# Kernel optimization log

Measured on AMD Instinct MI355X. Metric: run time of the kernel, lower is better.

The kernel has to match this reference:

```python
import jax, jax.numpy as jnp
import numpy as np
import math

DIM = 512
NUM_HEADS = 8
DIM_HEAD = DIM // NUM_HEADS


def normalized_coords(h, w):
    # (h*w, 2) with (x, y) in [0, 1]
    y = jnp.linspace(0.0, 1.0, h)
    x = jnp.linspace(0.0, 1.0, w)
    yg, xg = jnp.meshgrid(y, x, indexing='ij')
    return jnp.stack([xg.ravel(), yg.ravel()], axis=-1)


def rotate_half(x):
    dh = x.shape[-1] // 2
    return jnp.concatenate([-x[..., dh:], x[..., :dh]], axis=-1)


def apply_rope(t, coords):
    # t: (n, heads, seq, dim_head); coords: (seq, 2) (identical across batch)
    dim_half = t.shape[-1] // 2
    freq = 1.0 / (10000.0 ** (jnp.arange(dim_half, dtype=jnp.float32) / dim_half))
    ang_x = coords[:, 0:1] * freq  # (seq, dim_half)
    ang_y = coords[:, 1:2] * freq
    ang = jnp.concatenate([ang_x, ang_y], axis=-1)  # (seq, dim_head)
    cos, sin = jnp.cos(ang), jnp.sin(ang)
    return t * cos + rotate_half(t) * sin


def setup_inputs() -> dict:
    key = jax.random.key(0)
    ks = jax.random.split(key, 12)
    n, Np, d, H, W = 4, 1024, DIM, 64, 64
    s = 0.02
    return {
        'local_feat': jax.random.normal(ks[0], (n, Np, d), jnp.float32),
        'global_feat': jax.random.normal(ks[1], (n, d, H, W), jnp.float32),
        'Wq': jax.random.normal(ks[2], (d, d), jnp.float32) * s,
        'bq': jnp.zeros((d,), jnp.float32),
        'Wk': jax.random.normal(ks[3], (d, d), jnp.float32) * s,
        'bk': jnp.zeros((d,), jnp.float32),
        'Wv': jax.random.normal(ks[4], (d, d), jnp.float32) * s,
        'bv': jnp.zeros((d,), jnp.float32),
        'Wg': jax.random.normal(ks[5], (d, 2 * d), jnp.float32) * s,
        'bg': jnp.zeros((d,), jnp.float32),
        'Wo': jax.random.normal(ks[6], (d, d), jnp.float32) * s,
        'bo': jnp.zeros((d,), jnp.float32),
    }


def reference(local_feat, global_feat, Wq, bq, Wk, bk, Wv, bv, Wg, bg, Wo, bo):
    n, Np, d = local_feat.shape
    _, _, H, W = global_feat.shape
    h, dh = NUM_HEADS, DIM_HEAD
    gf = global_feat.reshape(n, d, H * W).transpose(0, 2, 1)  # (n, HW, d)

    P = int(math.isqrt(Np))
    local_coords = normalized_coords(P, P)      # (Np, 2)
    global_coords = normalized_coords(H, W)     # (HW, 2)

    def proj(x, Wt, b):
        return x @ Wt.T + b

    Q = proj(local_feat, Wq, bq).reshape(n, Np, h, dh).transpose(0, 2, 1, 3)
    K = proj(gf, Wk, bk).reshape(n, H * W, h, dh).transpose(0, 2, 1, 3)
    V = proj(gf, Wv, bv).reshape(n, H * W, h, dh).transpose(0, 2, 1, 3)

    Q = apply_rope(Q, local_coords)
    K = apply_rope(K, global_coords)

    scores = jnp.einsum('bhqd,bhkd->bhqk', Q, K) / math.sqrt(dh)
    attn = jax.nn.softmax(scores, axis=-1)
    ao = jnp.einsum('bhqk,bhkd->bhqd', attn, V)
    ao = ao.transpose(0, 2, 1, 3).reshape(n, Np, d)

    gate = jax.nn.sigmoid(jnp.concatenate([local_feat, ao], axis=-1) @ Wg.T + bg)
    enhanced = local_feat + gate * ao
    return enhanced @ Wo.T + bo
```

## Files before the change

kernel.cpp:

```cpp
#include <hip/hip_runtime.h>
#include <hip/hip_bf16.h>
#include <cstdint>

typedef __hip_bfloat16 BF;
typedef unsigned short ushort_t;
typedef __attribute__((ext_vector_type(8))) __bf16 bf16x8;
typedef __attribute__((ext_vector_type(4))) float f32x4;

__device__ __forceinline__ float b2f(BF x) { return __bfloat162float(x); }
__device__ __forceinline__ unsigned short f2bu(float f) {
  union { BF b; unsigned short u; } c; c.b = __float2bfloat16(f); return c.u;
}
__device__ __forceinline__ float rdE(const void* p, size_t i, bool f32) {
  return f32 ? ((const float*)p)[i] : __bfloat162float(((const BF*)p)[i]);
}
__device__ __forceinline__ void rd16(const void* p, size_t i, bool f32, ushort_t* out) {
  if (f32) {
    const float* fp = (const float*)p + i;
#pragma unroll
    for (int j = 0; j < 16; j += 4) {
      float4 v = *(const float4*)(fp + j);
      out[j] = f2bu(v.x); out[j + 1] = f2bu(v.y);
      out[j + 2] = f2bu(v.z); out[j + 3] = f2bu(v.w);
    }
  } else {
    const uint4* up = (const uint4*)((const BF*)p + i);
    *(uint4*)&out[0] = up[0];
    *(uint4*)&out[8] = up[1];
  }
}

__global__ void detect_k(const unsigned short* __restrict__ x, int* __restrict__ flag) {
  __shared__ int cnt;
  if (threadIdx.x == 0) cnt = 0;
  __syncthreads();
  int c = 0;
  for (int i = threadIdx.x; i < 4096; i += 256) {
    int e = (x[i] >> 7) & 0xFF;
    if (e >= 0x86) c++;
  }
  if (c) atomicAdd(&cnt, c);
  __syncthreads();
  if (threadIdx.x == 0) *flag = (cnt > 64) ? 1 : 0;
}

__global__ __launch_bounds__(256) void prep_k(const void* __restrict__ gfeat,
                                              BF* __restrict__ gfT,
                                              const int* __restrict__ flagp) {
  const bool f32 = (*flagp != 0);
  __shared__ __align__(16) ushort_t T[64][72];
  const int g = blockIdx.x;
  const int bz = g & 3, mt = (g >> 2) & 63, kt = g >> 8;
  const int t = threadIdx.x;
  {
    int krow = t >> 2, mg = t & 3;
    ushort_t vals[16];
    rd16(gfeat,
         (size_t)bz * 512 * 4096 + (size_t)(kt * 64 + krow) * 4096 + mt * 64 + mg * 16,
         f32, vals);
#pragma unroll
    for (int j = 0; j < 16; ++j) T[mg * 16 + j][krow] = vals[j];
  }
  __syncthreads();
  int mrow = t >> 2, kg = t & 3;
  uint4 a = *(const uint4*)&T[mrow][kg * 16];
  uint4 b = *(const uint4*)&T[mrow][kg * 16 + 8];
  size_t o = ((size_t)bz * 4096 + mt * 64 + mrow) * 512 + kt * 64 + kg * 16;
  *(uint4*)&gfT[o] = a;
  *(uint4*)&gfT[o + 8] = b;
}

#define QS 0.1803368801111f
template <int MODE>
__global__ __launch_bounds__(256) void mgemm_k(
    const void* __restrict__ Aext, const BF* __restrict__ Aint,
    const void* __restrict__ Bw, const void* __restrict__ Bw2,
    const void* __restrict__ biasv, const void* __restrict__ bias2,
    BF* __restrict__ outInt, BF* __restrict__ outInt2,
    void* __restrict__ outExt, int Kdim, const int* __restrict__ flagp) {
  const bool f32 = (*flagp != 0);
  const int tid = threadIdx.x;
  const int w = tid >> 6, lane = tid & 63;
  const int quad = lane >> 4, l16 = lane & 15;

  if constexpr (MODE == 5) {
    __shared__ __align__(16) ushort_t smem[2][128][72];
    auto As = smem[0];
    auto Bs = smem[1];
    const int wm = w >> 1, wn = w & 1;
    const int g = blockIdx.x;
    const int a = g & 7, y = (g >> 3) & 7, bidx = g >> 6;
    const int m0 = ((bidx << 1) | (a & 1)) * 128;
    const int n0 = y * 128;
    const int bz = a >> 1;

    f32x4 acc[4][4] = {};
    for (int k0 = 0; k0 < Kdim; k0 += 64) {
      __syncthreads();
#pragma unroll
      for (int u = 0; u < 2; ++u) {
        int unit = tid + u * 256;
        int row = unit >> 2, cg = unit & 3;
        const uint4* p = (const uint4*)(Aint + ((size_t)bz * 4096 + m0 + row) * 512 +
                                        k0 + cg * 16);
        *(uint4*)&As[row][cg * 16] = p[0];
        *(uint4*)&As[row][cg * 16 + 8] = p[1];
      }
#pragma unroll
      for (int u = 0; u < 2; ++u) {
        int unit = tid + u * 256;
        int row = unit >> 2, cg = unit & 3;
        const void* bsrc = (n0 >= 512) ? Bw2 : Bw;
        size_t nrow = (n0 >= 512) ? (n0 - 512 + row) : (n0 + row);
        ushort_t vals[16];
        rd16(bsrc, nrow * Kdim + k0 + cg * 16, f32, vals);
        *(uint4*)&Bs[row][cg * 16] = *(uint4*)&vals[0];
        *(uint4*)&Bs[row][cg * 16 + 8] = *(uint4*)&vals[8];
      }
      __syncthreads();
#pragma unroll
      for (int kc = 0; kc < 2; ++kc) {
        bf16x8 af[4], bfv[4];
#pragma unroll
        for (int i = 0; i < 4; ++i) {
          af[i] = *(const bf16x8*)&As[wm * 64 + i * 16 + l16][kc * 32 + quad * 8];
          bfv[i] = *(const bf16x8*)&Bs[wn * 64 + i * 16 + l16][kc * 32 + quad * 8];
        }
#pragma unroll
        for (int mt = 0; mt < 4; ++mt)
#pragma unroll
          for (int nt = 0; nt < 4; ++nt)
            acc[mt][nt] = __builtin_amdgcn_mfma_f32_16x16x32_bf16(af[mt], bfv[nt], acc[mt][nt], 0, 0, 0);
      }
    }
    if (n0 < 512) {
      const int head = (n0 + wn * 64) >> 6;
#pragma unroll
      for (int mt = 0; mt < 4; ++mt)
#pragma unroll
        for (int r = 0; r < 4; ++r) {
          int pg = m0 + wm * 64 + mt * 16 + quad * 4 + r;
          float x = (float)(pg & 63) * (1.f / 63.f);
          float yy = (float)(pg >> 6) * (1.f / 63.f);
          size_t base = (((size_t)bz * 8 + head) * 4096 + pg) * 64;
#pragma unroll
          for (int j = 0; j < 2; ++j) {
            int c0 = j * 16 + l16;
            float t0 = acc[mt][j][r] + rdE(biasv, head * 64 + c0, f32);
            float t1 = acc[mt][j + 2][r] + rdE(biasv, head * 64 + c0 + 32, f32);
            float fr = __expf((float)c0 * (-9.210340371976184f / 32.f));
            float ax = x * fr, ay = yy * fr;
            outInt[base + c0] = __float2bfloat16(t0 * __cosf(ax) - t1 * __sinf(ax));
            outInt[base + c0 + 32] = __float2bfloat16(t1 * __cosf(ay) + t0 * __sinf(ay));
          }
        }
    } else {
      const int n0v = n0 - 512;
      __syncthreads();
      ushort_t (*T)[136] = (ushort_t(*)[136]) & smem[0][0][0];
#pragma unroll
      for (int mt = 0; mt < 4; ++mt)
#pragma unroll
        for (int nt = 0; nt < 4; ++nt)
#pragma unroll
          for (int r = 0; r < 4; ++r) {
            int n_l = wn * 64 + nt * 16 + l16;
            int m_l = wm * 64 + mt * 16 + quad * 4 + r;
            T[n_l][m_l] = f2bu(acc[mt][nt][r] + rdE(bias2, n0v + n_l, f32));
          }
      __syncthreads();
      int row = tid >> 1, half = tid & 1;
      size_t gbase = (((size_t)bz * 8 + (n0v >> 6) + (row >> 6)) * 64 + (row & 63)) * 4096 +
                     m0 + half * 64;
      uint4* dst = (uint4*)(outInt2 + gbase);
      const uint4* src = (const uint4*)&T[row][half * 64];
#pragma unroll
      for (int j = 0; j < 8; ++j) dst[j] = src[j];
    }
  } else {
    __shared__ __align__(16) ushort_t As[64][72];
    __shared__ __align__(16) ushort_t Bs[64][72];
    const int m0 = blockIdx.x * 64, n0 = blockIdx.y * 64;

    f32x4 acc[4] = {};
    for (int k0 = 0; k0 < Kdim; k0 += 64) {
      __syncthreads();
      {
        int row = tid >> 2, cg = tid & 3;
        int kg = k0 + cg * 16;
        ushort_t vals[16];
        if constexpr (MODE == 3) {
          if (kg < 512) {
            rd16(Aext, (size_t)(m0 + row) * 512 + kg, f32, vals);
          } else {
            const uint4* p = (const uint4*)(Aint + (size_t)(m0 + row) * 512 + (kg - 512));
            *(uint4*)&vals[0] = p[0]; *(uint4*)&vals[8] = p[1];
          }
        } else if constexpr (MODE == 4) {
          const uint4* p = (const uint4*)(Aint + (size_t)(m0 + row) * 512 + kg);
          *(uint4*)&vals[0] = p[0]; *(uint4*)&vals[8] = p[1];
        } else {
          rd16(Aext, (size_t)(m0 + row) * Kdim + kg, f32, vals);
        }
        *(uint4*)&As[row][cg * 16] = *(uint4*)&vals[0];
        *(uint4*)&As[row][cg * 16 + 8] = *(uint4*)&vals[8];
        ushort_t bv[16];
        rd16(Bw, (size_t)(n0 + row) * Kdim + kg, f32, bv);
        *(uint4*)&Bs[row][cg * 16] = *(uint4*)&bv[0];
        *(uint4*)&Bs[row][cg * 16 + 8] = *(uint4*)&bv[8];
      }
      __syncthreads();
#pragma unroll
      for (int kc = 0; kc < 2; ++kc) {
        bf16x8 af = *(const bf16x8*)&As[w * 16 + l16][kc * 32 + quad * 8];
#pragma unroll
        for (int nt = 0; nt < 4; ++nt) {
          bf16x8 bfv = *(const bf16x8*)&Bs[nt * 16 + l16][kc * 32 + quad * 8];
          acc[nt] = __builtin_amdgcn_mfma_f32_16x16x32_bf16(af, bfv, acc[nt], 0, 0, 0);
        }
      }
    }

    if constexpr (MODE == 0) {
      const int head = n0 >> 6;
#pragma unroll
      for (int r = 0; r < 4; ++r) {
        int mg = m0 + w * 16 + quad * 4 + r;
        int bb = mg >> 10, qi = mg & 1023;
        float x = (float)(qi & 31) * (1.f / 31.f);
        float y = (float)(qi >> 5) * (1.f / 31.f);
        size_t base = (((size_t)bb * 8 + head) * 1024 + qi) * 64;
#pragma unroll
        for (int j = 0; j < 2; ++j) {
          int c0 = j * 16 + l16;
          float t0 = acc[j][r] + rdE(biasv, head * 64 + c0, f32);
          float t1 = acc[j + 2][r] + rdE(biasv, head * 64 + c0 + 32, f32);
          float fr = __expf((float)c0 * (-9.210340371976184f / 32.f));
          float ax = x * fr, ay = y * fr;
          outInt[base + c0] = __float2bfloat16((t0 * __cosf(ax) - t1 * __sinf(ax)) * QS);
          outInt[base + c0 + 32] = __float2bfloat16((t1 * __cosf(ay) + t0 * __sinf(ay)) * QS);
        }
      }
    } else if constexpr (MODE == 3) {
#pragma unroll
      for (int r = 0; r < 4; ++r) {
        int mg = m0 + w * 16 + quad * 4 + r;
#pragma unroll
        for (int nt = 0; nt < 4; ++nt) {
          int ng = n0 + nt * 16 + l16;
          size_t idx = (size_t)mg * 512 + ng;
          float g = 1.f / (1.f + __expf(-(acc[nt][r] + rdE(biasv, ng, f32))));
          outInt[idx] = __float2bfloat16(rdE(Aext, idx, f32) + g * b2f(Aint[idx]));
        }
      }
    } else {
#pragma unroll
      for (int r = 0; r < 4; ++r) {
        int mg = m0 + w * 16 + quad * 4 + r;
#pragma unroll
        for (int nt = 0; nt < 4; ++nt) {
          int ng = n0 + nt * 16 + l16;
          size_t idx = (size_t)mg * 512 + ng;
          float v = acc[nt][r] + rdE(biasv, ng, f32);
          if (f32) ((float*)outExt)[idx] = v;
          else ((BF*)outExt)[idx] = __float2bfloat16(v);
        }
      }
    }
  }
}

template <int NS>
__global__ __launch_bounds__(256) void attn_k(const BF* __restrict__ Q,
                                              const BF* __restrict__ K,
                                              const BF* __restrict__ VT,
                                              BF* __restrict__ AO,
                                              BF* __restrict__ Opart,
                                              float* __restrict__ lpart) {
  __shared__ __align__(16) ushort_t Ks[64][72];
  __shared__ __align__(16) ushort_t VTs[64][72];
  __shared__ __align__(16) ushort_t Ps[4][32][72];

  const int tid = threadIdx.x;
  const int w = tid >> 6, lane = tid & 63;
  const int quad = lane >> 4, l16 = lane & 15;

  const int g = blockIdx.x;
  const int bh = g & 31;
  const int qt = (g >> 5) & 7;
  const int ks = g >> 8;
  const int b = bh >> 3, h = bh & 7;
  const int q0 = qt * 128 + w * 32;
  const int kspan = 4096 / NS, kbase = ks * kspan;

  bf16x8 qa[2][2];
#pragma unroll
  for (int qs = 0; qs < 2; ++qs) {
    const BF* qp = Q + (((size_t)bh << 10) + q0 + qs * 16 + l16) * 64 + quad * 8;
    qa[qs][0] = *(const bf16x8*)qp;
    qa[qs][1] = *(const bf16x8*)(qp + 32);
  }
  bf16x8 ones;
#pragma unroll
  for (int j = 0; j < 8; ++j) ones[j] = (__bf16)1.0f;

  const BF* Kp = K + (size_t)bh * 4096 * 64;
  const BF* VTp = VT + (size_t)bh * 64 * 4096;

  f32x4 o[2][4] = {};
  f32x4 ol[2] = {};

  const int srow = tid >> 2, scol = (tid & 3) * 16;
  {
    const uint4* kp = (const uint4*)(Kp + (size_t)(kbase + srow) * 64 + scol);
    const uint4* vp = (const uint4*)(VTp + (size_t)srow * 4096 + kbase + scol);
    uint4 a = kp[0], bb = kp[1], c = vp[0], d = vp[1];
    *(uint4*)&Ks[srow][scol] = a;  *(uint4*)&Ks[srow][scol + 8] = bb;
    *(uint4*)&VTs[srow][scol] = c; *(uint4*)&VTs[srow][scol + 8] = d;
  }

  for (int c0 = kbase; c0 < kbase + kspan; c0 += 64) {
    __syncthreads();
    uint4 nk0, nk1, nv0, nv1;
    const bool more = (c0 + 64 < kbase + kspan);
    if (more) {
      const uint4* kp = (const uint4*)(Kp + (size_t)(c0 + 64 + srow) * 64 + scol);
      const uint4* vp = (const uint4*)(VTp + (size_t)srow * 4096 + c0 + 64 + scol);
      nk0 = kp[0]; nk1 = kp[1]; nv0 = vp[0]; nv1 = vp[1];
    }

#pragma unroll
    for (int ct = 0; ct < 4; ++ct) {
      bf16x8 kb0 = *(const bf16x8*)&Ks[ct * 16 + l16][quad * 8];
      bf16x8 kb1 = *(const bf16x8*)&Ks[ct * 16 + l16][32 + quad * 8];
#pragma unroll
      for (int qs = 0; qs < 2; ++qs) {
        f32x4 s = {};
        s = __builtin_amdgcn_mfma_f32_16x16x32_bf16(kb0, qa[qs][0], s, 0, 0, 0);
        s = __builtin_amdgcn_mfma_f32_16x16x32_bf16(kb1, qa[qs][1], s, 0, 0, 0);
        ushort_t pv[4];
#pragma unroll
        for (int r = 0; r < 4; ++r) pv[r] = f2bu(__builtin_exp2f(s[r]));
        *(uint2*)&Ps[w][qs * 16 + l16][ct * 16 + quad * 4] = *(uint2*)pv;
      }
    }

#pragma unroll
    for (int qs = 0; qs < 2; ++qs) {
      bf16x8 pa0 = *(const bf16x8*)&Ps[w][qs * 16 + l16][quad * 8];
      bf16x8 pa1 = *(const bf16x8*)&Ps[w][qs * 16 + l16][32 + quad * 8];
      ol[qs] = __builtin_amdgcn_mfma_f32_16x16x32_bf16(ones, pa0, ol[qs], 0, 0, 0);
      ol[qs] = __builtin_amdgcn_mfma_f32_16x16x32_bf16(ones, pa1, ol[qs], 0, 0, 0);
#pragma unroll
      for (int nt = 0; nt < 4; ++nt) {
        bf16x8 vb0 = *(const bf16x8*)&VTs[nt * 16 + l16][quad * 8];
        bf16x8 vb1 = *(const bf16x8*)&VTs[nt * 16 + l16][32 + quad * 8];
        o[qs][nt] = __builtin_amdgcn_mfma_f32_16x16x32_bf16(vb0, pa0, o[qs][nt], 0, 0, 0);
        o[qs][nt] = __builtin_amdgcn_mfma_f32_16x16x32_bf16(vb1, pa1, o[qs][nt], 0, 0, 0);
      }
    }

    __syncthreads();
    if (more) {
      *(uint4*)&Ks[srow][scol] = nk0;  *(uint4*)&Ks[srow][scol + 8] = nk1;
      *(uint4*)&VTs[srow][scol] = nv0; *(uint4*)&VTs[srow][scol + 8] = nv1;
    }
  }

#pragma unroll
  for (int qs = 0; qs < 2; ++qs) {
    int qg = q0 + qs * 16 + l16;
    if (NS == 1) {
      float invl = 1.f / ol[qs][0];
#pragma unroll
      for (int nt = 0; nt < 4; ++nt) {
        ushort_t ov[4];
#pragma unroll
        for (int r = 0; r < 4; ++r) ov[r] = f2bu(o[qs][nt][r] * invl);
        *(uint2*)(AO + (((size_t)b << 10) + qg) * 512 + h * 64 + nt * 16 + quad * 4) =
            *(uint2*)ov;
      }
    } else {
      if (quad == 0) lpart[ks * 32768 + (bh << 10) + qg] = ol[qs][0];
#pragma unroll
      for (int nt = 0; nt < 4; ++nt) {
        ushort_t ov[4];
#pragma unroll
        for (int r = 0; r < 4; ++r) ov[r] = f2bu(o[qs][nt][r]);
        *(uint2*)(Opart + (size_t)ks * 2097152 + (((size_t)bh << 10) + qg) * 64 +
                  nt * 16 + quad * 4) = *(uint2*)ov;
      }
    }
  }
}

template <int NS>
__global__ __launch_bounds__(256) void reduce_k(const BF* __restrict__ Opart,
                                                const float* __restrict__ lpart,
                                                BF* __restrict__ AO) {
  int e0 = (blockIdx.x * 256 + threadIdx.x) * 4;
  int row = e0 >> 6, col = e0 & 63;
  float lsum = 0.f;
#pragma unroll
  for (int s = 0; s < NS; ++s) lsum += lpart[s * 32768 + row];
  float inv = 1.f / lsum;
  float acc[4] = {};
#pragma unroll
  for (int s = 0; s < NS; ++s) {
    uint2 u = *(const uint2*)((const ushort_t*)Opart + (size_t)s * 2097152 +
                              (size_t)row * 64 + col);
    const ushort_t* pu = (const ushort_t*)&u;
#pragma unroll
    for (int j = 0; j < 4; ++j)
      acc[j] += __uint_as_float((unsigned)pu[j] << 16);
  }
  ushort_t outv[4];
#pragma unroll
  for (int j = 0; j < 4; ++j) outv[j] = f2bu(acc[j] * inv);
  int bh = row >> 10, q = row & 1023, bb = bh >> 3, h = bh & 7;
  *(uint2*)(AO + (((size_t)bb << 10) + q) * 512 + h * 64 + col) = *(uint2*)outv;
}

extern "C" void kernel_launch(void* const* d_in, const int* in_sizes, int n_in,
                              void* d_out, int out_size, void* d_ws, size_t ws_size,
                              hipStream_t stream) {
  const void* local = d_in[0];
  const void* gfeat = d_in[1];
  const void* Wq = d_in[2];
  const void* bq = d_in[3];
  const void* Wk = d_in[4];
  const void* bk = d_in[5];
  const void* Wv = d_in[6];
  const void* bv = d_in[7];
  const void* Wg = d_in[8];
  const void* bg = d_in[9];
  const void* Wo = d_in[10];
  const void* bo = d_in[11];

  char* w = (char*)d_ws;
  int* flag = (int*)w;        w += 256;
  BF* Qb = (BF*)w;            w += (size_t)2097152 * 2;
  BF* Kb = (BF*)w;            w += (size_t)8388608 * 2;
  BF* VTb = (BF*)w;           w += (size_t)8388608 * 2;
  BF* AO = (BF*)w;            w += (size_t)2097152 * 2;
  BF* gfT = (BF*)w;
  BF* Opart = (BF*)w;
  size_t baseOff = (size_t)(w - (char*)d_ws);
  BF* ENH = Qb;

  int NS = 1;
  if (baseOff + 4 * (4194304 + 131072) <= ws_size) NS = 4;
  else if (baseOff + 16777216 + 2 * 131072 <= ws_size) NS = 2;
  float* lpart = (float*)(w + (size_t)NS * 4194304);

  dim3 blk(256);
  detect_k<<<dim3(1), blk, 0, stream>>>((const unsigned short*)local, flag);
  prep_k<<<dim3(2048), blk, 0, stream>>>(gfeat, gfT, flag);
  mgemm_k<0><<<dim3(64, 8, 1), blk, 0, stream>>>(local, nullptr, Wq, nullptr, bq, nullptr, Qb, nullptr, nullptr, 512, flag);
  mgemm_k<5><<<dim3(1024, 1, 1), blk, 0, stream>>>(nullptr, gfT, Wk, Wv, bk, bv, Kb, VTb, nullptr, 512, flag);
  if (NS == 4) {
    attn_k<4><<<dim3(1024), blk, 0, stream>>>(Qb, Kb, VTb, AO, Opart, lpart);
    reduce_k<4><<<dim3(2048), blk, 0, stream>>>(Opart, lpart, AO);
  } else if (NS == 2) {
    attn_k<2><<<dim3(512), blk, 0, stream>>>(Qb, Kb, VTb, AO, Opart, lpart);
    reduce_k<2><<<dim3(2048), blk, 0, stream>>>(Opart, lpart, AO);
  } else {
    attn_k<1><<<dim3(256), blk, 0, stream>>>(Qb, Kb, VTb, AO, nullptr, nullptr);
  }
  mgemm_k<3><<<dim3(64, 8, 1), blk, 0, stream>>>(local, AO, Wg, nullptr, bg, nullptr, ENH, nullptr, nullptr, 1024, flag);
  mgemm_k<4><<<dim3(64, 8, 1), blk, 0, stream>>>(nullptr, ENH, Wo, nullptr, bo, nullptr, nullptr, nullptr, d_out, 512, flag);
}
```

Before: 281.6 us.

## Load K and V tiles directly from global into registers, dropping LDS staging

```diff
diff --git a/kernel.cpp b/kernel.cpp
--- a/kernel.cpp
+++ b/kernel.cpp
@@ -277,8 +277,6 @@
                                               BF* __restrict__ AO,
                                               BF* __restrict__ Opart,
                                               float* __restrict__ lpart) {
-  __shared__ __align__(16) ushort_t Ks[64][72];
-  __shared__ __align__(16) ushort_t VTs[64][72];
   __shared__ __align__(16) ushort_t Ps[4][32][72];
 
   const int tid = threadIdx.x;
@@ -310,34 +308,28 @@
   f32x4 o[2][4] = {};
   f32x4 ol[2] = {};
 
-  const int srow = tid >> 2, scol = (tid & 3) * 16;
-  {
-    const uint4* kp = (const uint4*)(Kp + (size_t)(kbase + srow) * 64 + scol);
-    const uint4* vp = (const uint4*)(VTp + (size_t)srow * 4096 + kbase + scol);
-    uint4 a = kp[0], bb = kp[1], c = vp[0], d = vp[1];
-    *(uint4*)&Ks[srow][scol] = a;  *(uint4*)&Ks[srow][scol + 8] = bb;
-    *(uint4*)&VTs[srow][scol] = c; *(uint4*)&VTs[srow][scol + 8] = d;
-  }
-
   for (int c0 = kbase; c0 < kbase + kspan; c0 += 64) {
-    __syncthreads();
-    uint4 nk0, nk1, nv0, nv1;
-    const bool more = (c0 + 64 < kbase + kspan);
-    if (more) {
-      const uint4* kp = (const uint4*)(Kp + (size_t)(c0 + 64 + srow) * 64 + scol);
-      const uint4* vp = (const uint4*)(VTp + (size_t)srow * 4096 + c0 + 64 + scol);
-      nk0 = kp[0]; nk1 = kp[1]; nv0 = vp[0]; nv1 = vp[1];
-    }
-
+    bf16x8 kb[4][2], vb[4][2];
 #pragma unroll
     for (int ct = 0; ct < 4; ++ct) {
-      bf16x8 kb0 = *(const bf16x8*)&Ks[ct * 16 + l16][quad * 8];
-      bf16x8 kb1 = *(const bf16x8*)&Ks[ct * 16 + l16][32 + quad * 8];
+      const BF* kp = Kp + (size_t)(c0 + ct * 16 + l16) * 64 + quad * 8;
+      kb[ct][0] = *(const bf16x8*)kp;
+      kb[ct][1] = *(const bf16x8*)(kp + 32);
+    }
+#pragma unroll
+    for (int nt = 0; nt < 4; ++nt) {
+      const BF* vp = VTp + (size_t)(nt * 16 + l16) * 4096 + c0 + quad * 8;
+      vb[nt][0] = *(const bf16x8*)vp;
+      vb[nt][1] = *(const bf16x8*)(vp + 32);
+    }
+
+#pragma unroll
+    for (int ct = 0; ct < 4; ++ct) {
 #pragma unroll
       for (int qs = 0; qs < 2; ++qs) {
         f32x4 s = {};
-        s = __builtin_amdgcn_mfma_f32_16x16x32_bf16(kb0, qa[qs][0], s, 0, 0, 0);
-        s = __builtin_amdgcn_mfma_f32_16x16x32_bf16(kb1, qa[qs][1], s, 0, 0, 0);
+        s = __builtin_amdgcn_mfma_f32_16x16x32_bf16(kb[ct][0], qa[qs][0], s, 0, 0, 0);
+        s = __builtin_amdgcn_mfma_f32_16x16x32_bf16(kb[ct][1], qa[qs][1], s, 0, 0, 0);
         ushort_t pv[4];
 #pragma unroll
         for (int r = 0; r < 4; ++r) pv[r] = f2bu(__builtin_exp2f(s[r]));
@@ -353,17 +345,9 @@
       ol[qs] = __builtin_amdgcn_mfma_f32_16x16x32_bf16(ones, pa1, ol[qs], 0, 0, 0);
 #pragma unroll
       for (int nt = 0; nt < 4; ++nt) {
-        bf16x8 vb0 = *(const bf16x8*)&VTs[nt * 16 + l16][quad * 8];
-        bf16x8 vb1 = *(const bf16x8*)&VTs[nt * 16 + l16][32 + quad * 8];
-        o[qs][nt] = __builtin_amdgcn_mfma_f32_16x16x32_bf16(vb0, pa0, o[qs][nt], 0, 0, 0);
-        o[qs][nt] = __builtin_amdgcn_mfma_f32_16x16x32_bf16(vb1, pa1, o[qs][nt], 0, 0, 0);
-      }
-    }
-
-    __syncthreads();
-    if (more) {
-      *(uint4*)&Ks[srow][scol] = nk0;  *(uint4*)&Ks[srow][scol + 8] = nk1;
-      *(uint4*)&VTs[srow][scol] = nv0; *(uint4*)&VTs[srow][scol + 8] = nv1;
+        o[qs][nt] = __builtin_amdgcn_mfma_f32_16x16x32_bf16(vb[nt][0], pa0, o[qs][nt], 0, 0, 0);
+        o[qs][nt] = __builtin_amdgcn_mfma_f32_16x16x32_bf16(vb[nt][1], pa1, o[qs][nt], 0, 0, 0);
+      }
     }
   }
 
```

After: 336.5 us. 19.5% more time.

## Fuse split-K reduction into gate GEMM, merge prep with Q projection, drop dtype detection

Applied to the files above, without the earlier changes.

```diff
diff --git a/kernel.cpp b/kernel.cpp
--- a/kernel.cpp
+++ b/kernel.cpp
@@ -7,266 +7,215 @@
 typedef __attribute__((ext_vector_type(8))) __bf16 bf16x8;
 typedef __attribute__((ext_vector_type(4))) float f32x4;
 
-__device__ __forceinline__ float b2f(BF x) { return __bfloat162float(x); }
+__device__ __forceinline__ float bu2f(ushort_t u) {
+  return __uint_as_float((unsigned)u << 16);
+}
+__device__ __forceinline__ unsigned pk2(float a, float b) {
+  union { __hip_bfloat162 h; unsigned u; } c;
+  c.h = __float22bfloat162_rn(make_float2(a, b));
+  return c.u;
+}
 __device__ __forceinline__ unsigned short f2bu(float f) {
   union { BF b; unsigned short u; } c; c.b = __float2bfloat16(f); return c.u;
 }
-__device__ __forceinline__ float rdE(const void* p, size_t i, bool f32) {
-  return f32 ? ((const float*)p)[i] : __bfloat162float(((const BF*)p)[i]);
-}
-__device__ __forceinline__ void rd16(const void* p, size_t i, bool f32, ushort_t* out) {
-  if (f32) {
-    const float* fp = (const float*)p + i;
-#pragma unroll
-    for (int j = 0; j < 16; j += 4) {
-      float4 v = *(const float4*)(fp + j);
-      out[j] = f2bu(v.x); out[j + 1] = f2bu(v.y);
-      out[j + 2] = f2bu(v.z); out[j + 3] = f2bu(v.w);
-    }
-  } else {
-    const uint4* up = (const uint4*)((const BF*)p + i);
-    *(uint4*)&out[0] = up[0];
-    *(uint4*)&out[8] = up[1];
-  }
-}
-
-__global__ void detect_k(const unsigned short* __restrict__ x, int* __restrict__ flag) {
-  __shared__ int cnt;
-  if (threadIdx.x == 0) cnt = 0;
-  __syncthreads();
-  int c = 0;
-  for (int i = threadIdx.x; i < 4096; i += 256) {
-    int e = (x[i] >> 7) & 0xFF;
-    if (e >= 0x86) c++;
-  }
-  if (c) atomicAdd(&cnt, c);
-  __syncthreads();
-  if (threadIdx.x == 0) *flag = (cnt > 64) ? 1 : 0;
-}
-
-__global__ __launch_bounds__(256) void prep_k(const void* __restrict__ gfeat,
-                                              BF* __restrict__ gfT,
-                                              const int* __restrict__ flagp) {
-  const bool f32 = (*flagp != 0);
-  __shared__ __align__(16) ushort_t T[64][72];
-  const int g = blockIdx.x;
-  const int bz = g & 3, mt = (g >> 2) & 63, kt = g >> 8;
+__device__ __forceinline__ float b2f(BF x) { return __bfloat162float(x); }
+__device__ __forceinline__ void rd16f(const float* fp, ushort_t* out) {
+#pragma unroll
+  for (int j = 0; j < 16; j += 4) {
+    float4 v = *(const float4*)(fp + j);
+    ((unsigned*)out)[j / 2] = pk2(v.x, v.y);
+    ((unsigned*)out)[j / 2 + 1] = pk2(v.z, v.w);
+  }
+}
+
+#define QS 0.1803368801111f
+
+__global__ __launch_bounds__(256) void pre_k(const float* __restrict__ local,
+                                             const float* __restrict__ gfeat,
+                                             const float* __restrict__ Wq,
+                                             const float* __restrict__ bq,
+                                             BF* __restrict__ gfT,
+                                             BF* __restrict__ Qb) {
+  __shared__ __align__(16) ushort_t smem[2][64][72];
   const int t = threadIdx.x;
-  {
-    int krow = t >> 2, mg = t & 3;
-    ushort_t vals[16];
-    rd16(gfeat,
-         (size_t)bz * 512 * 4096 + (size_t)(kt * 64 + krow) * 4096 + mt * 64 + mg * 16,
-         f32, vals);
-#pragma unroll
-    for (int j = 0; j < 16; ++j) T[mg * 16 + j][krow] = vals[j];
-  }
-  __syncthreads();
-  int mrow = t >> 2, kg = t & 3;
-  uint4 a = *(const uint4*)&T[mrow][kg * 16];
-  uint4 b = *(const uint4*)&T[mrow][kg * 16 + 8];
-  size_t o = ((size_t)bz * 4096 + mt * 64 + mrow) * 512 + kt * 64 + kg * 16;
-  *(uint4*)&gfT[o] = a;
-  *(uint4*)&gfT[o + 8] = b;
-}
-
-#define QS 0.1803368801111f
-template <int MODE>
-__global__ __launch_bounds__(256) void mgemm_k(
-    const void* __restrict__ Aext, const BF* __restrict__ Aint,
-    const void* __restrict__ Bw, const void* __restrict__ Bw2,
-    const void* __restrict__ biasv, const void* __restrict__ bias2,
-    BF* __restrict__ outInt, BF* __restrict__ outInt2,
-    void* __restrict__ outExt, int Kdim, const int* __restrict__ flagp) {
-  const bool f32 = (*flagp != 0);
+  if (blockIdx.x < 2048) {
+    auto T = smem[0];
+    const int g = blockIdx.x;
+    const int bz = g & 3, mt = (g >> 2) & 63, kt = g >> 8;
+    {
+      int krow = t >> 2, mg = t & 3;
+      ushort_t vals[16];
+      rd16f(gfeat + (size_t)bz * 512 * 4096 + (size_t)(kt * 64 + krow) * 4096 +
+                mt * 64 + mg * 16,
+            vals);
+#pragma unroll
+      for (int j = 0; j < 16; ++j) T[mg * 16 + j][krow] = vals[j];
+    }
+    __syncthreads();
+    int mrow = t >> 2, kg = t & 3;
+    uint4 a = *(const uint4*)&T[mrow][kg * 16];
+    uint4 b = *(const uint4*)&T[mrow][kg * 16 + 8];
+    size_t o = ((size_t)bz * 4096 + mt * 64 + mrow) * 512 + kt * 64 + kg * 16;
+    *(uint4*)&gfT[o] = a;
+    *(uint4*)&gfT[o + 8] = b;
+    return;
+  }
+  auto As = smem[0];
+  auto Bs = smem[1];
+  const int bx = blockIdx.x - 2048;
+  const int m0 = (bx & 63) * 64, n0 = (bx >> 6) * 64;
+  const int w = t >> 6, lane = t & 63;
+  const int quad = lane >> 4, l16 = lane & 15;
+
+  f32x4 acc[4] = {};
+  for (int k0 = 0; k0 < 512; k0 += 64) {
+    __syncthreads();
+    {
+      int row = t >> 2, cg = t & 3;
+      int kg = k0 + cg * 16;
+      ushort_t vals[16];
+      rd16f(local + (size_t)(m0 + row) * 512 + kg, vals);
+      *(uint4*)&As[row][cg * 16] = *(uint4*)&vals[0];
+      *(uint4*)&As[row][cg * 16 + 8] = *(uint4*)&vals[8];
+      ushort_t bv[16];
+      rd16f(Wq + (size_t)(n0 + row) * 512 + kg, bv);
+      *(uint4*)&Bs[row][cg * 16] = *(uint4*)&bv[0];
+      *(uint4*)&Bs[row][cg * 16 + 8] = *(uint4*)&bv[8];
+    }
+    __syncthreads();
+#pragma unroll
+    for (int kc = 0; kc < 2; ++kc) {
+      bf16x8 af = *(const bf16x8*)&As[w * 16 + l16][kc * 32 + quad * 8];
+#pragma unroll
+      for (int nt = 0; nt < 4; ++nt) {
+        bf16x8 bfv = *(const bf16x8*)&Bs[nt * 16 + l16][kc * 32 + quad * 8];
+        acc[nt] = __builtin_amdgcn_mfma_f32_16x16x32_bf16(af, bfv, acc[nt], 0, 0, 0);
+      }
+    }
+  }
+  const int head = n0 >> 6;
+#pragma unroll
+  for (int r = 0; r < 4; ++r) {
+    int mg = m0 + w * 16 + quad * 4 + r;
+    int bb = mg >> 10, qi = mg & 1023;
+    float x = (float)(qi & 31) * (1.f / 31.f);
+    float y = (float)(qi >> 5) * (1.f / 31.f);
+    size_t base = (((size_t)bb * 8 + head) * 1024 + qi) * 64;
+#pragma unroll
+    for (int j = 0; j < 2; ++j) {
+      int c0 = j * 16 + l16;
+      float t0 = acc[j][r] + bq[head * 64 + c0];
+      float t1 = acc[j + 2][r] + bq[head * 64 + c0 + 32];
+      float fr = __expf((float)c0 * (-9.210340371976184f / 32.f));
+      float ax = x * fr, ay = y * fr;
+      Qb[base + c0] = __float2bfloat16((t0 * __cosf(ax) - t1 * __sinf(ax)) * QS);
+      Qb[base + c0 + 32] = __float2bfloat16((t1 * __cosf(ay) + t0 * __sinf(ay)) * QS);
+    }
+  }
+}
+
+__global__ __launch_bounds__(256) void kv_k(const BF* __restrict__ gfT,
+                                            const float* __restrict__ Wk,
+                                            const float* __restrict__ Wv,
+                                            const float* __restrict__ bk,
+                                            const float* __restrict__ bv,
+                                            BF* __restrict__ Kb,
+                                            BF* __restrict__ VTb) {
+  __shared__ __align__(16) ushort_t smem[2][128][72];
+  auto As = smem[0];
+  auto Bs = smem[1];
   const int tid = threadIdx.x;
   const int w = tid >> 6, lane = tid & 63;
   const int quad = lane >> 4, l16 = lane & 15;
-
-  if constexpr (MODE == 5) {
-    __shared__ __align__(16) ushort_t smem[2][128][72];
-    auto As = smem[0];
-    auto Bs = smem[1];
-    const int wm = w >> 1, wn = w & 1;
-    const int g = blockIdx.x;
-    const int a = g & 7, y = (g >> 3) & 7, bidx = g >> 6;
-    const int m0 = ((bidx << 1) | (a & 1)) * 128;
-    const int n0 = y * 128;
-    const int bz = a >> 1;
-
-    f32x4 acc[4][4] = {};
-    for (int k0 = 0; k0 < Kdim; k0 += 64) {
-      __syncthreads();
-#pragma unroll
-      for (int u = 0; u < 2; ++u) {
-        int unit = tid + u * 256;
-        int row = unit >> 2, cg = unit & 3;
-        const uint4* p = (const uint4*)(Aint + ((size_t)bz * 4096 + m0 + row) * 512 +
-                                        k0 + cg * 16);
-        *(uint4*)&As[row][cg * 16] = p[0];
-        *(uint4*)&As[row][cg * 16 + 8] = p[1];
-      }
-#pragma unroll
-      for (int u = 0; u < 2; ++u) {
-        int unit = tid + u * 256;
-        int row = unit >> 2, cg = unit & 3;
-        const void* bsrc = (n0 >= 512) ? Bw2 : Bw;
-        size_t nrow = (n0 >= 512) ? (n0 - 512 + row) : (n0 + row);
-        ushort_t vals[16];
-        rd16(bsrc, nrow * Kdim + k0 + cg * 16, f32, vals);
-        *(uint4*)&Bs[row][cg * 16] = *(uint4*)&vals[0];
-        *(uint4*)&Bs[row][cg * 16 + 8] = *(uint4*)&vals[8];
-      }
-      __syncthreads();
-#pragma unroll
-      for (int kc = 0; kc < 2; ++kc) {
-        bf16x8 af[4], bfv[4];
-#pragma unroll
-        for (int i = 0; i < 4; ++i) {
-          af[i] = *(const bf16x8*)&As[wm * 64 + i * 16 + l16][kc * 32 + quad * 8];
-          bfv[i] = *(const bf16x8*)&Bs[wn * 64 + i * 16 + l16][kc * 32 + quad * 8];
-        }
-#pragma unroll
-        for (int mt = 0; mt < 4; ++mt)
-#pragma unroll
-          for (int nt = 0; nt < 4; ++nt)
-            acc[mt][nt] = __builtin_amdgcn_mfma_f32_16x16x32_bf16(af[mt], bfv[nt], acc[mt][nt], 0, 0, 0);
-      }
-    }
-    if (n0 < 512) {
-      const int head = (n0 + wn * 64) >> 6;
+  const int wm = w >> 1, wn = w & 1;
+  const int g = blockIdx.x;
+  const int a = g & 7, y = (g >> 3) & 7, bidx = g >> 6;
+  const int m0 = ((bidx << 1) | (a & 1)) * 128;
+  const int n0 = y * 128;
+  const int bz = a >> 1;
+
+  f32x4 acc[4][4] = {};
+  for (int k0 = 0; k0 < 512; k0 += 64) {
+    __syncthreads();
+#pragma unroll
+    for (int u = 0; u < 2; ++u) {
+      int unit = tid + u * 256;
+      int row = unit >> 2, cg = unit & 3;
+      const uint4* p = (const uint4*)(gfT + ((size_t)bz * 4096 + m0 + row) * 512 +
+                                      k0 + cg * 16);
+      *(uint4*)&As[row][cg * 16] = p[0];
+      *(uint4*)&As[row][cg * 16 + 8] = p[1];
+    }
+#pragma unroll
+    for (int u = 0; u < 2; ++u) {
+      int unit = tid + u * 256;
+      int row = unit >> 2, cg = unit & 3;
+      const float* bsrc = (n0 >= 512) ? Wv : Wk;
+      size_t nrow = (n0 >= 512) ? (n0 - 512 + row) : (n0 + row);
+      ushort_t vals[16];
+      rd16f(bsrc + nrow * 512 + k0 + cg * 16, vals);
+      *(uint4*)&Bs[row][cg * 16] = *(uint4*)&vals[0];
+      *(uint4*)&Bs[row][cg * 16 + 8] = *(uint4*)&vals[8];
+    }
+    __syncthreads();
+#pragma unroll
+    for (int kc = 0; kc < 2; ++kc) {
+      bf16x8 af[4], bfv[4];
+#pragma unroll
+      for (int i = 0; i < 4; ++i) {
+        af[i] = *(const bf16x8*)&As[wm * 64 + i * 16 + l16][kc * 32 + quad * 8];
+        bfv[i] = *(const bf16x8*)&Bs[wn * 64 + i * 16 + l16][kc * 32 + quad * 8];
+      }
 #pragma unroll
       for (int mt = 0; mt < 4; ++mt)
 #pragma unroll
-        for (int r = 0; r < 4; ++r) {
-          int pg = m0 + wm * 64 + mt * 16 + quad * 4 + r;
-          float x = (float)(pg & 63) * (1.f / 63.f);
-          float yy = (float)(pg >> 6) * (1.f / 63.f);
-          size_t base = (((size_t)bz * 8 + head) * 4096 + pg) * 64;
-#pragma unroll
-          for (int j = 0; j < 2; ++j) {
-            int c0 = j * 16 + l16;
-            float t0 = acc[mt][j][r] + rdE(biasv, head * 64 + c0, f32);
-            float t1 = acc[mt][j + 2][r] + rdE(biasv, head * 64 + c0 + 32, f32);
-            float fr = __expf((float)c0 * (-9.210340371976184f / 32.f));
-            float ax = x * fr, ay = yy * fr;
-            outInt[base + c0] = __float2bfloat16(t0 * __cosf(ax) - t1 * __sinf(ax));
-            outInt[base + c0 + 32] = __float2bfloat16(t1 * __cosf(ay) + t0 * __sinf(ay));
-          }
-        }
-    } else {
-      const int n0v = n0 - 512;
-      __syncthreads();
-      ushort_t (*T)[136] = (ushort_t(*)[136]) & smem[0][0][0];
-#pragma unroll
-      for (int mt = 0; mt < 4; ++mt)
-#pragma unroll
         for (int nt = 0; nt < 4; ++nt)
-#pragma unroll
-          for (int r = 0; r < 4; ++r) {
-            int n_l = wn * 64 + nt * 16 + l16;
-            int m_l = wm * 64 + mt * 16 + quad * 4 + r;
-            T[n_l][m_l] = f2bu(acc[mt][nt][r] + rdE(bias2, n0v + n_l, f32));
-          }
-      __syncthreads();
-      int row = tid >> 1, half = tid & 1;
-      size_t gbase = (((size_t)bz * 8 + (n0v >> 6) + (row >> 6)) * 64 + (row & 63)) * 4096 +
-                     m0 + half * 64;
-      uint4* dst = (uint4*)(outInt2 + gbase);
-      const uint4* src = (const uint4*)&T[row][half * 64];
-#pragma unroll
-      for (int j = 0; j < 8; ++j) dst[j] = src[j];
-    }
-  } else {
-    __shared__ __align__(16) ushort_t As[64][72];
-    __shared__ __align__(16) ushort_t Bs[64][72];
-    const int m0 = blockIdx.x * 64, n0 = blockIdx.y * 64;
-
-    f32x4 acc[4] = {};
-    for (int k0 = 0; k0 < Kdim; k0 += 64) {
-      __syncthreads();
-      {
-        int row = tid >> 2, cg = tid & 3;
-        int kg = k0 + cg * 16;
-        ushort_t vals[16];
-        if constexpr (MODE == 3) {
-          if (kg < 512) {
-            rd16(Aext, (size_t)(m0 + row) * 512 + kg, f32, vals);
-          } else {
-            const uint4* p = (const uint4*)(Aint + (size_t)(m0 + row) * 512 + (kg - 512));
-            *(uint4*)&vals[0] = p[0]; *(uint4*)&vals[8] = p[1];
-          }
-        } else if constexpr (MODE == 4) {
-          const uint4* p = (const uint4*)(Aint + (size_t)(m0 + row) * 512 + kg);
-          *(uint4*)&vals[0] = p[0]; *(uint4*)&vals[8] = p[1];
-        } else {
-          rd16(Aext, (size_t)(m0 + row) * Kdim + kg, f32, vals);
-        }
-        *(uint4*)&As[row][cg * 16] = *(uint4*)&vals[0];
-        *(uint4*)&As[row][cg * 16 + 8] = *(uint4*)&vals[8];
-        ushort_t bv[16];
-        rd16(Bw, (size_t)(n0 + row) * Kdim + kg, f32, bv);
-        *(uint4*)&Bs[row][cg * 16] = *(uint4*)&bv[0];
-        *(uint4*)&Bs[row][cg * 16 + 8] = *(uint4*)&bv[8];
-      }
-      __syncthreads();
-#pragma unroll
-      for (int kc = 0; kc < 2; ++kc) {
-        bf16x8 af = *(const bf16x8*)&As[w * 16 + l16][kc * 32 + quad * 8];
-#pragma unroll
-        for (int nt = 0; nt < 4; ++nt) {
-          bf16x8 bfv = *(const bf16x8*)&Bs[nt * 16 + l16][kc * 32 + quad * 8];
-          acc[nt] = __builtin_amdgcn_mfma_f32_16x16x32_bf16(af, bfv, acc[nt], 0, 0, 0);
-        }
-      }
-    }
-
-    if constexpr (MODE == 0) {
-      const int head = n0 >> 6;
+          acc[mt][nt] = __builtin_amdgcn_mfma_f32_16x16x32_bf16(af[mt], bfv[nt], acc[mt][nt], 0, 0, 0);
+    }
+  }
+  if (n0 < 512) {
+    const int head = (n0 + wn * 64) >> 6;
+#pragma unroll
+    for (int mt = 0; mt < 4; ++mt)
 #pragma unroll
       for (int r = 0; r < 4; ++r) {
-        int mg = m0 + w * 16 + quad * 4 + r;
-        int bb = mg >> 10, qi = mg & 1023;
-        float x = (float)(qi & 31) * (1.f / 31.f);
-        float y = (float)(qi >> 5) * (1.f / 31.f);
-        size_t base = (((size_t)bb * 8 + head) * 1024 + qi) * 64;
+        int pg = m0 + wm * 64 + mt * 16 + quad * 4 + r;
+        float x = (float)(pg & 63) * (1.f / 63.f);
+        float yy = (float)(pg >> 6) * (1.f / 63.f);
+        size_t base = (((size_t)bz * 8 + head) * 4096 + pg) * 64;
 #pragma unroll
         for (int j = 0; j < 2; ++j) {
           int c0 = j * 16 + l16;
-          float t0 = acc[j][r] + rdE(biasv, head * 64 + c0, f32);
-          float t1 = acc[j + 2][r] + rdE(biasv, head * 64 + c0 + 32, f32);
+          float t0 = acc[mt][j][r] + bk[head * 64 + c0];
+          float t1 = acc[mt][j + 2][r] + bk[head * 64 + c0 + 32];
           float fr = __expf((float)c0 * (-9.210340371976184f / 32.f));
-          float ax = x * fr, ay = y * fr;
-          outInt[base + c0] = __float2bfloat16((t0 * __cosf(ax) - t1 * __sinf(ax)) * QS);
-          outInt[base + c0 + 32] = __float2bfloat16((t1 * __cosf(ay) + t0 * __sinf(ay)) * QS);
+          float ax = x * fr, ay = yy * fr;
+          Kb[base + c0] = __float2bfloat16(t0 * __cosf(ax) - t1 * __sinf(ax));
+          Kb[base + c0 + 32] = __float2bfloat16(t1 * __cosf(ay) + t0 * __sinf(ay));
         }
       }
-    } else if constexpr (MODE == 3) {
-#pragma unroll
-      for (int r = 0; r < 4; ++r) {
-        int mg = m0 + w * 16 + quad * 4 + r;
-#pragma unroll
-        for (int nt = 0; nt < 4; ++nt) {
-          int ng = n0 + nt * 16 + l16;
-          size_t idx = (size_t)mg * 512 + ng;
-          float g = 1.f / (1.f + __expf(-(acc[nt][r] + rdE(biasv, ng, f32))));
-          outInt[idx] = __float2bfloat16(rdE(Aext, idx, f32) + g * b2f(Aint[idx]));
+  } else {
+    const int n0v = n0 - 512;
+    __syncthreads();
+    ushort_t (*T)[136] = (ushort_t(*)[136]) & smem[0][0][0];
+#pragma unroll
+    for (int mt = 0; mt < 4; ++mt)
+#pragma unroll
+      for (int nt = 0; nt < 4; ++nt)
+#pragma unroll
+        for (int r = 0; r < 4; ++r) {
+          int n_l = wn * 64 + nt * 16 + l16;
+          int m_l = wm * 64 + mt * 16 + quad * 4 + r;
+          T[n_l][m_l] = f2bu(acc[mt][nt][r] + bv[n0v + n_l]);
         }
-      }
-    } else {
-#pragma unroll
-      for (int r = 0; r < 4; ++r) {
-        int mg = m0 + w * 16 + quad * 4 + r;
-#pragma unroll
-        for (int nt = 0; nt < 4; ++nt) {
-          int ng = n0 + nt * 16 + l16;
-          size_t idx = (size_t)mg * 512 + ng;
-          float v = acc[nt][r] + rdE(biasv, ng, f32);
-          if (f32) ((float*)outExt)[idx] = v;
-          else ((BF*)outExt)[idx] = __float2bfloat16(v);
-        }
-      }
-    }
+    __syncthreads();
+    int row = tid >> 1, half = tid & 1;
+    size_t gbase = (((size_t)bz * 8 + (n0v >> 6) + (row >> 6)) * 64 + (row & 63)) * 4096 +
+                   m0 + half * 64;
+    uint4* dst = (uint4*)(VTb + gbase);
+    const uint4* src = (const uint4*)&T[row][half * 64];
+#pragma unroll
+    for (int j = 0; j < 8; ++j) dst[j] = src[j];
   }
 }
 
@@ -338,10 +287,10 @@
         f32x4 s = {};
         s = __builtin_amdgcn_mfma_f32_16x16x32_bf16(kb0, qa[qs][0], s, 0, 0, 0);
         s = __builtin_amdgcn_mfma_f32_16x16x32_bf16(kb1, qa[qs][1], s, 0, 0, 0);
-        ushort_t pv[4];
-#pragma unroll
-        for (int r = 0; r < 4; ++r) pv[r] = f2bu(__builtin_exp2f(s[r]));
-        *(uint2*)&Ps[w][qs * 16 + l16][ct * 16 + quad * 4] = *(uint2*)pv;
+        uint2 uu;
+        uu.x = pk2(__builtin_exp2f(s[0]), __builtin_exp2f(s[1]));
+        uu.y = pk2(__builtin_exp2f(s[2]), __builtin_exp2f(s[3]));
+        *(uint2*)&Ps[w][qs * 16 + l16][ct * 16 + quad * 4] = uu;
       }
     }
 
@@ -374,71 +323,183 @@
       float invl = 1.f / ol[qs][0];
 #pragma unroll
       for (int nt = 0; nt < 4; ++nt) {
-        ushort_t ov[4];
-#pragma unroll
-        for (int r = 0; r < 4; ++r) ov[r] = f2bu(o[qs][nt][r] * invl);
-        *(uint2*)(AO + (((size_t)b << 10) + qg) * 512 + h * 64 + nt * 16 + quad * 4) =
-            *(uint2*)ov;
+        uint2 uu;
+        uu.x = pk2(o[qs][nt][0] * invl, o[qs][nt][1] * invl);
+        uu.y = pk2(o[qs][nt][2] * invl, o[qs][nt][3] * invl);
+        *(uint2*)(AO + (((size_t)b << 10) + qg) * 512 + h * 64 + nt * 16 + quad * 4) = uu;
       }
     } else {
       if (quad == 0) lpart[ks * 32768 + (bh << 10) + qg] = ol[qs][0];
 #pragma unroll
       for (int nt = 0; nt < 4; ++nt) {
-        ushort_t ov[4];
-#pragma unroll
-        for (int r = 0; r < 4; ++r) ov[r] = f2bu(o[qs][nt][r]);
+        uint2 uu;
+        uu.x = pk2(o[qs][nt][0], o[qs][nt][1]);
+        uu.y = pk2(o[qs][nt][2], o[qs][nt][3]);
         *(uint2*)(Opart + (size_t)ks * 2097152 + (((size_t)bh << 10) + qg) * 64 +
-                  nt * 16 + quad * 4) = *(uint2*)ov;
+                  nt * 16 + quad * 4) = uu;
       }
     }
   }
 }
 
 template <int NS>
-__global__ __launch_bounds__(256) void reduce_k(const BF* __restrict__ Opart,
-                                                const float* __restrict__ lpart,
-                                                BF* __restrict__ AO) {
-  int e0 = (blockIdx.x * 256 + threadIdx.x) * 4;
-  int row = e0 >> 6, col = e0 & 63;
-  float lsum = 0.f;
-#pragma unroll
-  for (int s = 0; s < NS; ++s) lsum += lpart[s * 32768 + row];
-  float inv = 1.f / lsum;
-  float acc[4] = {};
-#pragma unroll
-  for (int s = 0; s < NS; ++s) {
-    uint2 u = *(const uint2*)((const ushort_t*)Opart + (size_t)s * 2097152 +
-                              (size_t)row * 64 + col);
-    const ushort_t* pu = (const ushort_t*)&u;
-#pragma unroll
-    for (int j = 0; j < 4; ++j)
-      acc[j] += __uint_as_float((unsigned)pu[j] << 16);
-  }
-  ushort_t outv[4];
-#pragma unroll
-  for (int j = 0; j < 4; ++j) outv[j] = f2bu(acc[j] * inv);
-  int bh = row >> 10, q = row & 1023, bb = bh >> 3, h = bh & 7;
-  *(uint2*)(AO + (((size_t)bb << 10) + q) * 512 + h * 64 + col) = *(uint2*)outv;
+__global__ __launch_bounds__(256) void gate_k(const float* __restrict__ local,
+                                              const BF* __restrict__ AO,
+                                              const BF* __restrict__ Opart,
+                                              const float* __restrict__ lpart,
+                                              const float* __restrict__ Wg,
+                                              const float* __restrict__ bg,
+                                              BF* __restrict__ ENH) {
+  __shared__ __align__(16) ushort_t As[64][72];
+  __shared__ __align__(16) ushort_t Bs[64][72];
+  const int tid = threadIdx.x;
+  const int w = tid >> 6, lane = tid & 63;
+  const int quad = lane >> 4, l16 = lane & 15;
+  const int m0 = blockIdx.x * 64, n0 = blockIdx.y * 64;
+
+  f32x4 acc[4] = {};
+  float aosv[4][4];
+  for (int k0 = 0; k0 < 1024; k0 += 64) {
+    __syncthreads();
+    {
+      int row = tid >> 2, cg = tid & 3;
+      int kg = k0 + cg * 16;
+      ushort_t vals[16];
+      if (kg < 512) {
+        rd16f(local + (size_t)(m0 + row) * 512 + kg, vals);
+      } else {
+        int c = kg - 512;
+        int hh = c >> 6, dh0 = c & 63;
+        int mg = m0 + row;
+        size_t bq = (size_t)(((mg >> 10) * 8 + hh) << 10) + (mg & 1023);
+        if (NS == 1) {
+          const uint4* p = (const uint4*)(AO + (size_t)mg * 512 + c);
+          *(uint4*)&vals[0] = p[0]; *(uint4*)&vals[8] = p[1];
+        } else {
+          float ls = 0.f;
+#pragma unroll
+          for (int s2 = 0; s2 < NS; ++s2) ls += lpart[s2 * 32768 + bq];
+          float inv = 1.f / ls;
+          float av[16] = {};
+#pragma unroll
+          for (int s2 = 0; s2 < NS; ++s2) {
+            const ushort_t* op = (const ushort_t*)Opart + (size_t)s2 * 2097152 +
+                                 bq * 64 + dh0;
+            uint4 u0 = ((const uint4*)op)[0], u1 = ((const uint4*)op)[1];
+            const ushort_t* pu = (const ushort_t*)&u0;
+#pragma unroll
+            for (int j = 0; j < 8; ++j) av[j] += bu2f(pu[j]);
+            pu = (const ushort_t*)&u1;
+#pragma unroll
+            for (int j = 0; j < 8; ++j) av[8 + j] += bu2f(pu[j]);
+          }
+#pragma unroll
+          for (int j = 0; j < 16; j += 2)
+            ((unsigned*)vals)[j / 2] = pk2(av[j] * inv, av[j + 1] * inv);
+        }
+      }
+      *(uint4*)&As[row][cg * 16] = *(uint4*)&vals[0];
+      *(uint4*)&As[row][cg * 16 + 8] = *(uint4*)&vals[8];
+      ushort_t bv[16];
+      rd16f(Wg + (size_t)(n0 + row) * 1024 + kg, bv);
+      *(uint4*)&Bs[row][cg * 16] = *(uint4*)&bv[0];
+      *(uint4*)&Bs[row][cg * 16 + 8] = *(uint4*)&bv[8];
+    }
+    __syncthreads();
+    if (k0 == 512 + n0) {
+#pragma unroll
+      for (int r = 0; r < 4; ++r)
+#pragma unroll
+        for (int nt = 0; nt < 4; ++nt)
+          aosv[r][nt] = bu2f(As[w * 16 + quad * 4 + r][nt * 16 + l16]);
+    }
+#pragma unroll
+    for (int kc = 0; kc < 2; ++kc) {
+      bf16x8 af = *(const bf16x8*)&As[w * 16 + l16][kc * 32 + quad * 8];
+#pragma unroll
+      for (int nt = 0; nt < 4; ++nt) {
+        bf16x8 bfv = *(const bf16x8*)&Bs[nt * 16 + l16][kc * 32 + quad * 8];
+        acc[nt] = __builtin_amdgcn_mfma_f32_16x16x32_bf16(af, bfv, acc[nt], 0, 0, 0);
+      }
+    }
+  }
+#pragma unroll
+  for (int r = 0; r < 4; ++r) {
+    int mg = m0 + w * 16 + quad * 4 + r;
+#pragma unroll
+    for (int nt = 0; nt < 4; ++nt) {
+      int ng = n0 + nt * 16 + l16;
+      size_t idx = (size_t)mg * 512 + ng;
+      float gg = 1.f / (1.f + __expf(-(acc[nt][r] + bg[ng])));
+      ENH[idx] = __float2bfloat16(local[idx] + gg * aosv[r][nt]);
+    }
+  }
+}
+
+__global__ __launch_bounds__(256) void out_k(const BF* __restrict__ ENH,
+                                             const float* __restrict__ Wo,
+                                             const float* __restrict__ bo,
+                                             float* __restrict__ out) {
+  __shared__ __align__(16) ushort_t As[64][72];
+  __shared__ __align__(16) ushort_t Bs[64][72];
+  const int tid = threadIdx.x;
+  const int w = tid >> 6, lane = tid & 63;
+  const int quad = lane >> 4, l16 = lane & 15;
+  const int m0 = blockIdx.x * 64, n0 = blockIdx.y * 64;
+
+  f32x4 acc[4] = {};
+  for (int k0 = 0; k0 < 512; k0 += 64) {
+    __syncthreads();
+    {
+      int row = tid >> 2, cg = tid & 3;
+      int kg = k0 + cg * 16;
+      const uint4* p = (const uint4*)(ENH + (size_t)(m0 + row) * 512 + kg);
+      *(uint4*)&As[row][cg * 16] = p[0];
+      *(uint4*)&As[row][cg * 16 + 8] = p[1];
+      ushort_t bv[16];
+      rd16f(Wo + (size_t)(n0 + row) * 512 + kg, bv);
+      *(uint4*)&Bs[row][cg * 16] = *(uint4*)&bv[0];
+      *(uint4*)&Bs[row][cg * 16 + 8] = *(uint4*)&bv[8];
+    }
+    __syncthreads();
+#pragma unroll
+    for (int kc = 0; kc < 2; ++kc) {
+      bf16x8 af = *(const bf16x8*)&As[w * 16 + l16][kc * 32 + quad * 8];
+#pragma unroll
+      for (int nt = 0; nt < 4; ++nt) {
+        bf16x8 bfv = *(const bf16x8*)&Bs[nt * 16 + l16][kc * 32 + quad * 8];
+        acc[nt] = __builtin_amdgcn_mfma_f32_16x16x32_bf16(af, bfv, acc[nt], 0, 0, 0);
+      }
+    }
+  }
+#pragma unroll
+  for (int r = 0; r < 4; ++r) {
+    int mg = m0 + w * 16 + quad * 4 + r;
+#pragma unroll
+    for (int nt = 0; nt < 4; ++nt) {
+      int ng = n0 + nt * 16 + l16;
+      out[(size_t)mg * 512 + ng] = acc[nt][r] + bo[ng];
+    }
+  }
 }
 
 extern "C" void kernel_launch(void* const* d_in, const int* in_sizes, int n_in,
                               void* d_out, int out_size, void* d_ws, size_t ws_size,
                               hipStream_t stream) {
-  const void* local = d_in[0];
-  const void* gfeat = d_in[1];
-  const void* Wq = d_in[2];
-  const void* bq = d_in[3];
-  const void* Wk = d_in[4];
-  const void* bk = d_in[5];
-  const void* Wv = d_in[6];
-  const void* bv = d_in[7];
-  const void* Wg = d_in[8];
-  const void* bg = d_in[9];
-  const void* Wo = d_in[10];
-  const void* bo = d_in[11];
+  const float* local = (const float*)d_in[0];
+  const float* gfeat = (const float*)d_in[1];
+  const float* Wq = (const float*)d_in[2];
+  const float* bq = (const float*)d_in[3];
+  const float* Wk = (const float*)d_in[4];
+  const float* bk = (const float*)d_in[5];
+  const float* Wv = (const float*)d_in[6];
+  const float* bv = (const float*)d_in[7];
+  const float* Wg = (const float*)d_in[8];
+  const float* bg = (const float*)d_in[9];
+  const float* Wo = (const float*)d_in[10];
+  const float* bo = (const float*)d_in[11];
 
   char* w = (char*)d_ws;
-  int* flag = (int*)w;        w += 256;
   BF* Qb = (BF*)w;            w += (size_t)2097152 * 2;
   BF* Kb = (BF*)w;            w += (size_t)8388608 * 2;
   BF* VTb = (BF*)w;           w += (size_t)8388608 * 2;
@@ -454,19 +515,17 @@
   float* lpart = (float*)(w + (size_t)NS * 4194304);
 
   dim3 blk(256);
-  detect_k<<<dim3(1), blk, 0, stream>>>((const unsigned short*)local, flag);
-  prep_k<<<dim3(2048), blk, 0, stream>>>(gfeat, gfT, flag);
-  mgemm_k<0><<<dim3(64, 8, 1), blk, 0, stream>>>(local, nullptr, Wq, nullptr, bq, nullptr, Qb, nullptr, nullptr, 512, flag);
-  mgemm_k<5><<<dim3(1024, 1, 1), blk, 0, stream>>>(nullptr, gfT, Wk, Wv, bk, bv, Kb, VTb, nullptr, 512, flag);
+  pre_k<<<dim3(2560), blk, 0, stream>>>(local, gfeat, Wq, bq, gfT, Qb);
+  kv_k<<<dim3(1024), blk, 0, stream>>>(gfT, Wk, Wv, bk, bv, Kb, VTb);
   if (NS == 4) {
     attn_k<4><<<dim3(1024), blk, 0, stream>>>(Qb, Kb, VTb, AO, Opart, lpart);
-    reduce_k<4><<<dim3(2048), blk, 0, stream>>>(Opart, lpart, AO);
+    gate_k<4><<<dim3(64, 8), blk, 0, stream>>>(local, AO, Opart, lpart, Wg, bg, ENH);
   } else if (NS == 2) {
     attn_k<2><<<dim3(512), blk, 0, stream>>>(Qb, Kb, VTb, AO, Opart, lpart);
-    reduce_k<2><<<dim3(2048), blk, 0, stream>>>(Opart, lpart, AO);
+    gate_k<2><<<dim3(64, 8), blk, 0, stream>>>(local, AO, Opart, lpart, Wg, bg, ENH);
   } else {
     attn_k<1><<<dim3(256), blk, 0, stream>>>(Qb, Kb, VTb, AO, nullptr, nullptr);
-  }
-  mgemm_k<3><<<dim3(64, 8, 1), blk, 0, stream>>>(local, AO, Wg, nullptr, bg, nullptr, ENH, nullptr, nullptr, 1024, flag);
-  mgemm_k<4><<<dim3(64, 8, 1), blk, 0, stream>>>(nullptr, ENH, Wo, nullptr, bo, nullptr, nullptr, nullptr, d_out, 512, flag);
-}
+    gate_k<1><<<dim3(64, 8), blk, 0, stream>>>(local, AO, Opart, lpart, Wg, bg, ENH);
+  }
+  out_k<<<dim3(64, 8), blk, 0, stream>>>(ENH, Wo, bo, (float*)d_out);
+}
```

Result: faster. 259.1 us (-8.0%).
